# Performance work log

Hardware: AMD Instinct MI355X
Metric: run time of the kernel (lower is better)

## Reference

```python
import jax, jax.numpy as jnp
import numpy as np

N, T, D = 64, 2048, 256


def setup_inputs() -> dict:
    key = jax.random.key(0)
    k1, k2, k3, k4 = jax.random.split(key, 4)
    query = jax.random.normal(k1, (N, D), dtype=jnp.float32)
    key_t = jax.random.normal(k2, (N, T, D), dtype=jnp.float32)
    value = jax.random.normal(k3, (N, T, D), dtype=jnp.float32)
    lens = jax.random.randint(k4, (N,), 1, T + 1, dtype=jnp.int64)  # valid lengths in [1, T]
    return {"query": query, "key": key_t, "value": value, "lens": lens}


def reference(query, key, value, lens):
    # energy[n, t] = <key[n, t, :], query[n, :]>
    energy = jnp.einsum("ntd,nd->nt", key, query)
    attention = jax.nn.softmax(energy, axis=1)  # [N, T]
    # mask out positions >= lens[n], then renormalize over valid positions
    attention_mask = (jnp.arange(T)[None, :] < lens[:, None]).astype(attention.dtype)
    mask_attention = attention * attention_mask
    norm_attention = mask_attention / jnp.sum(mask_attention, axis=1, keepdims=True)
    # context[n, d] = sum_t norm_attention[n, t] * value[n, t, d]
    context = jnp.einsum("nt,ntd->nd", norm_attention, value)
    return (context, norm_attention)
```

## Files before the change

### kernel.cpp

```cpp
#include <hip/hip_runtime.h>


#define N_B 64
#define T_S 2048
#define D_S 256
#define TPB 256
#define RC 64
#define NC (T_S / RC)

typedef __attribute__((ext_vector_type(4))) float f4;
typedef __attribute__((ext_vector_type(2))) float f2;

__device__ __forceinline__ f4 ntload4(const float* p) {
  return __builtin_nontemporal_load((const f4*)p);
}
__device__ __forceinline__ f4 fma4(float s, f4 a, f4 b) {
  b.x = fmaf(s, a.x, b.x);
  b.y = fmaf(s, a.y, b.y);
  b.z = fmaf(s, a.z, b.z);
  b.w = fmaf(s, a.w, b.w);
  return b;
}

__global__ __launch_bounds__(TPB) void fused_kernel(
    const float* __restrict__ q, const float* __restrict__ k,
    const float* __restrict__ v, const int* __restrict__ lens,
    float* __restrict__ p_out, float2* __restrict__ mzc,
    float* __restrict__ Oc) {
  const int n = blockIdx.y, c = blockIdx.x;
  const int L = lens[n];
  const int t0 = c * RC;
  if (t0 >= L) return;
  const int tend = min(t0 + RC, L);
  const int tid = threadIdx.x;
  const int lane = tid & 63, wave = tid >> 6;

  __shared__ f4 q_sh[64];
  __shared__ float e_sh[RC];
  __shared__ float p_sh[RC];
  __shared__ f4 part[TPB];

  if (tid < 64) q_sh[tid] = ((const f4*)(q + (size_t)n * D_S))[tid];
  if (tid < RC) e_sh[tid] = -1e30f;
  __syncthreads();

  {
    const int s = lane & 15, qd = lane >> 4;
    const float* kb = k + (size_t)n * T_S * D_S + s * 4;
    const int rbase = t0 + wave * 16 + qd;
#pragma unroll
    for (int g = 0; g < 4; ++g) {
      const int r = rbase + g * 4;
      const float* krow = kb + (size_t)r * D_S;
      float acc = 0.f;
#pragma unroll
      for (int i = 0; i < 4; ++i) {
        const f4 kv = ntload4(krow + i * 64);
        const f4 qv = q_sh[i * 16 + s];
        acc = fmaf(kv.x, qv.x, acc);
        acc = fmaf(kv.y, qv.y, acc);
        acc = fmaf(kv.z, qv.z, acc);
        acc = fmaf(kv.w, qv.w, acc);
      }
#pragma unroll
      for (int off = 8; off > 0; off >>= 1) acc += __shfl_xor(acc, off, 64);
      if (s == 0 && r < tend) e_sh[r - t0] = acc;
    }
  }
  __syncthreads();

  if (wave == 0) {
    const float e = e_sh[lane];
    float m = e;
#pragma unroll
    for (int off = 32; off > 0; off >>= 1) m = fmaxf(m, __shfl_xor(m, off, 64));
    const float pv = __expf(e - m);
    float z = pv;
#pragma unroll
    for (int off = 32; off > 0; off >>= 1) z += __shfl_xor(z, off, 64);
    p_sh[lane] = pv;
    p_out[(size_t)n * T_S + t0 + lane] = pv;
    if (lane == 0) mzc[n * NC + c] = make_float2(m, z);
  }
  __syncthreads();

  const int dg = tid & 63, tg = tid >> 6;
  const float* vb = v + (size_t)n * T_S * D_S + (size_t)t0 * D_S + dg * 4;
  f4 a0 = {0.f, 0.f, 0.f, 0.f}, a1 = a0, a2 = a0, a3 = a0;
#pragma unroll
  for (int j = 0; j < 4; ++j) {
    const int r0 = j * 16 + tg;
    const f4 v0 = ntload4(vb + (size_t)r0 * D_S);
    const f4 v1 = ntload4(vb + (size_t)(r0 + 4) * D_S);
    const f4 v2 = ntload4(vb + (size_t)(r0 + 8) * D_S);
    const f4 v3 = ntload4(vb + (size_t)(r0 + 12) * D_S);
    a0 = fma4(p_sh[r0], v0, a0);
    a1 = fma4(p_sh[r0 + 4], v1, a1);
    a2 = fma4(p_sh[r0 + 8], v2, a2);
    a3 = fma4(p_sh[r0 + 12], v3, a3);
  }
  part[tid] = (a0 + a1) + (a2 + a3);
  __syncthreads();
  if (tg == 0) {
    const f4 r = part[dg] + part[dg + 64] + part[dg + 128] + part[dg + 192];
    ((f4*)(Oc + ((size_t)(n * NC + c)) * D_S))[dg] = r;
  }
}

__global__ __launch_bounds__(TPB) void merge_kernel(
    const int* __restrict__ lens, const float* __restrict__ p_in,
    const float2* __restrict__ mzc, const float* __restrict__ Oc,
    float* __restrict__ out_ctx, float* __restrict__ out_attn) {
  const int n = blockIdx.y, cx = blockIdx.x;
  const int L = lens[n];
  const int nc = (L + RC - 1) / RC;
  const int tid = threadIdx.x;
  __shared__ float s_sh[NC];
  __shared__ float cpart[TPB];

  if (tid < 64) {
    float m = -1e30f, z = 0.f;
    if (tid < nc) {
      const float2 mz = mzc[n * NC + tid];
      m = mz.x;
      z = mz.y;
    }
    float M = m;
#pragma unroll
    for (int off = 32; off > 0; off >>= 1) M = fmaxf(M, __shfl_xor(M, off, 64));
    const float sc = __expf(m - M);
    float zs = z * sc;
#pragma unroll
    for (int off = 32; off > 0; off >>= 1) zs += __shfl_xor(zs, off, 64);
    if (tid < NC) s_sh[tid] = sc / zs;
  }
  __syncthreads();

  {
    const int t = cx * (T_S / 4) + tid * 2;
    const f2 p = *(const f2*)(p_in + (size_t)n * T_S + t);
    const float sc = s_sh[t >> 6];
    f2 a;
    a.x = (t < L) ? p.x * sc : 0.f;
    a.y = (t + 1 < L) ? p.y * sc : 0.f;
    *(f2*)(out_attn + (size_t)n * T_S + t) = a;
  }

  {
    const int d = cx * 64 + (tid & 63);
    const int cg = tid >> 6;
    const float* ob = Oc + (size_t)n * NC * D_S + d;
    float acc = 0.f;
#pragma unroll
    for (int kk = 0; kk < 8; ++kk) {
      const int cc = cg + kk * 4;
      acc = fmaf(s_sh[cc], ob[(size_t)cc * D_S], acc);
    }
    cpart[tid] = acc;
    __syncthreads();
    if (tid < 64)
      out_ctx[(size_t)n * D_S + d] =
          (cpart[tid] + cpart[tid + 64]) + (cpart[tid + 128] + cpart[tid + 192]);
  }
}

extern "C" void kernel_launch(void* const* d_in, const int* in_sizes, int n_in,
                              void* d_out, int out_size, void* d_ws,
                              size_t ws_size, hipStream_t stream) {
  const float* query = (const float*)d_in[0];
  const float* key = (const float*)d_in[1];
  const float* value = (const float*)d_in[2];
  const int* lens = (const int*)d_in[3];

  float* out_ctx = (float*)d_out;
  float* out_attn = (float*)d_out + N_B * D_S;

  float* p = (float*)d_ws;
  float2* mzc = (float2*)(p + (size_t)N_B * T_S);
  float* Oc = (float*)(mzc + N_B * NC);

  const dim3 grid1(NC, N_B);
  fused_kernel<<<grid1, TPB, 0, stream>>>(query, key, value, lens, p, mzc, Oc);
  const dim3 grid2(4, N_B);
  merge_kernel<<<grid2, TPB, 0, stream>>>(lens, p, mzc, Oc, out_ctx, out_attn);
}
```

Baseline: 242.7 us.

## Make each wave own a 16-row chunk with wave-local softmax, no LDS or barriers

The fused kernel now gives each wavefront its own 16-row time chunk. The chunk's energies, local max/sum and weighted V accumulation stay in registers and use shuffles, so shared memory and block barriers are gone. Rows past the valid length skip their K loads, and V rows whose weight is zero are skipped. In exchange there are four times as many partial chunks, so the merge kernel handles 128 chunk partials per batch, which adds workspace traffic and reduction work.

Result: slower. 257.6 us (+6.1%).

```diff
diff --git a/kernel.cpp b/kernel.cpp
--- a/kernel.cpp
+++ b/kernel.cpp
@@ -5,8 +5,8 @@
 #define T_S 2048
 #define D_S 256
 #define TPB 256
-#define RC 64
-#define NC (T_S / RC)
+#define RC 16
+#define NCH (T_S / RC)
 
 typedef __attribute__((ext_vector_type(4))) float f4;
 typedef __attribute__((ext_vector_type(2))) float f2;
@@ -27,84 +27,91 @@
     const float* __restrict__ v, const int* __restrict__ lens,
     float* __restrict__ p_out, float2* __restrict__ mzc,
     float* __restrict__ Oc) {
-  const int n = blockIdx.y, c = blockIdx.x;
+  const int n = blockIdx.y;
   const int L = lens[n];
-  const int t0 = c * RC;
-  if (t0 >= L) return;
-  const int tend = min(t0 + RC, L);
-  const int tid = threadIdx.x;
-  const int lane = tid & 63, wave = tid >> 6;
-
-  __shared__ f4 q_sh[64];
-  __shared__ float e_sh[RC];
-  __shared__ float p_sh[RC];
-  __shared__ f4 part[TPB];
-
-  if (tid < 64) q_sh[tid] = ((const f4*)(q + (size_t)n * D_S))[tid];
-  if (tid < RC) e_sh[tid] = -1e30f;
-  __syncthreads();
-
-  {
-    const int s = lane & 15, qd = lane >> 4;
-    const float* kb = k + (size_t)n * T_S * D_S + s * 4;
-    const int rbase = t0 + wave * 16 + qd;
-#pragma unroll
-    for (int g = 0; g < 4; ++g) {
-      const int r = rbase + g * 4;
-      const float* krow = kb + (size_t)r * D_S;
-      float acc = 0.f;
-#pragma unroll
-      for (int i = 0; i < 4; ++i) {
-        const f4 kv = ntload4(krow + i * 64);
-        const f4 qv = q_sh[i * 16 + s];
-        acc = fmaf(kv.x, qv.x, acc);
-        acc = fmaf(kv.y, qv.y, acc);
-        acc = fmaf(kv.z, qv.z, acc);
-        acc = fmaf(kv.w, qv.w, acc);
-      }
-#pragma unroll
-      for (int off = 8; off > 0; off >>= 1) acc += __shfl_xor(acc, off, 64);
-      if (s == 0 && r < tend) e_sh[r - t0] = acc;
-    }
-  }
-  __syncthreads();
-
-  if (wave == 0) {
-    const float e = e_sh[lane];
-    float m = e;
-#pragma unroll
-    for (int off = 32; off > 0; off >>= 1) m = fmaxf(m, __shfl_xor(m, off, 64));
-    const float pv = __expf(e - m);
-    float z = pv;
-#pragma unroll
-    for (int off = 32; off > 0; off >>= 1) z += __shfl_xor(z, off, 64);
-    p_sh[lane] = pv;
-    p_out[(size_t)n * T_S + t0 + lane] = pv;
-    if (lane == 0) mzc[n * NC + c] = make_float2(m, z);
-  }
-  __syncthreads();
-
-  const int dg = tid & 63, tg = tid >> 6;
-  const float* vb = v + (size_t)n * T_S * D_S + (size_t)t0 * D_S + dg * 4;
-  f4 a0 = {0.f, 0.f, 0.f, 0.f}, a1 = a0, a2 = a0, a3 = a0;
-#pragma unroll
-  for (int j = 0; j < 4; ++j) {
-    const int r0 = j * 16 + tg;
-    const f4 v0 = ntload4(vb + (size_t)r0 * D_S);
-    const f4 v1 = ntload4(vb + (size_t)(r0 + 4) * D_S);
-    const f4 v2 = ntload4(vb + (size_t)(r0 + 8) * D_S);
-    const f4 v3 = ntload4(vb + (size_t)(r0 + 12) * D_S);
-    a0 = fma4(p_sh[r0], v0, a0);
-    a1 = fma4(p_sh[r0 + 4], v1, a1);
-    a2 = fma4(p_sh[r0 + 8], v2, a2);
-    a3 = fma4(p_sh[r0 + 12], v3, a3);
-  }
-  part[tid] = (a0 + a1) + (a2 + a3);
-  __syncthreads();
-  if (tg == 0) {
-    const f4 r = part[dg] + part[dg + 64] + part[dg + 128] + part[dg + 192];
-    ((f4*)(Oc + ((size_t)(n * NC + c)) * D_S))[dg] = r;
-  }
+  const int wave = threadIdx.x >> 6, lane = threadIdx.x & 63;
+  const int c16 = blockIdx.x * 4 + wave;
+  const int r0 = c16 * RC;
+  if (r0 >= L) return;
+  const int tendw = min(r0 + RC, L);
+  const int s = lane & 15, qd = lane >> 4;
+
+  const f4* qp = (const f4*)(q + (size_t)n * D_S);
+  const f4 qv0 = qp[s], qv1 = qp[s + 16], qv2 = qp[s + 32], qv3 = qp[s + 48];
+
+  const float* kb = k + (size_t)n * T_S * D_S + s * 4;
+  float e0 = -1e30f, e1 = -1e30f, e2 = -1e30f, e3 = -1e30f;
+#define EROW(G, EV)                                                      \
+  {                                                                      \
+    const int r = r0 + qd + 4 * (G);                                     \
+    if (r < tendw) {                                                     \
+      const float* krow = kb + (size_t)r * D_S;                          \
+      const f4 k0 = ntload4(krow);                                       \
+      const f4 k1 = ntload4(krow + 64);                                  \
+      const f4 k2 = ntload4(krow + 128);                                 \
+      const f4 k3 = ntload4(krow + 192);                                 \
+      float a = k0.x * qv0.x;                                            \
+      a = fmaf(k0.y, qv0.y, a);                                          \
+      a = fmaf(k0.z, qv0.z, a);                                          \
+      a = fmaf(k0.w, qv0.w, a);                                          \
+      a = fmaf(k1.x, qv1.x, a);                                          \
+      a = fmaf(k1.y, qv1.y, a);                                          \
+      a = fmaf(k1.z, qv1.z, a);                                          \
+      a = fmaf(k1.w, qv1.w, a);                                          \
+      a = fmaf(k2.x, qv2.x, a);                                          \
+      a = fmaf(k2.y, qv2.y, a);                                          \
+      a = fmaf(k2.z, qv2.z, a);                                          \
+      a = fmaf(k2.w, qv2.w, a);                                          \
+      a = fmaf(k3.x, qv3.x, a);                                          \
+      a = fmaf(k3.y, qv3.y, a);                                          \
+      a = fmaf(k3.z, qv3.z, a);                                          \
+      a = fmaf(k3.w, qv3.w, a);                                          \
+      a += __shfl_xor(a, 8, 64);                                         \
+      a += __shfl_xor(a, 4, 64);                                         \
+      a += __shfl_xor(a, 2, 64);                                         \
+      a += __shfl_xor(a, 1, 64);                                         \
+      EV = a;                                                            \
+    }                                                                    \
+  }
+  EROW(0, e0)
+  EROW(1, e1)
+  EROW(2, e2)
+  EROW(3, e3)
+#undef EROW
+
+  float m = fmaxf(fmaxf(e0, e1), fmaxf(e2, e3));
+  m = fmaxf(m, __shfl_xor(m, 16, 64));
+  m = fmaxf(m, __shfl_xor(m, 32, 64));
+  const float p0 = __expf(e0 - m), p1 = __expf(e1 - m);
+  const float p2 = __expf(e2 - m), p3 = __expf(e3 - m);
+  float z = (p0 + p1) + (p2 + p3);
+  z += __shfl_xor(z, 16, 64);
+  z += __shfl_xor(z, 32, 64);
+
+  if (s < 4) {
+    float pv = p0;
+    pv = (s == 1) ? p1 : pv;
+    pv = (s == 2) ? p2 : pv;
+    pv = (s == 3) ? p3 : pv;
+    p_out[(size_t)n * T_S + r0 + qd + 4 * s] = pv;
+  }
+  if (lane == 0) mzc[n * NCH + c16] = make_float2(m, z);
+
+  const float* vb = v + (size_t)n * T_S * D_S + (size_t)r0 * D_S + lane * 4;
+  f4 aA = {0.f, 0.f, 0.f, 0.f}, aB = aA;
+#define VROW(G, Q2, ACC)                                                   \
+  {                                                                       \
+    const float sc = __shfl(p##G, (Q2)*16, 64);       \
+    if (sc != 0.f)                                                        \
+      ACC = fma4(sc, ntload4(vb + (size_t)((Q2) + 4 * (G)) * D_S), ACC);  \
+  }
+  VROW(0, 0, aA) VROW(0, 1, aB) VROW(0, 2, aA) VROW(0, 3, aB)
+  VROW(1, 0, aA) VROW(1, 1, aB) VROW(1, 2, aA) VROW(1, 3, aB)
+  VROW(2, 0, aA) VROW(2, 1, aB) VROW(2, 2, aA) VROW(2, 3, aB)
+  VROW(3, 0, aA) VROW(3, 1, aB) VROW(3, 2, aA) VROW(3, 3, aB)
+#undef VROW
+
+  ((f4*)(Oc + ((size_t)(n * NCH + c16)) * D_S))[lane] = aA + aB;
 }
 
 __global__ __launch_bounds__(TPB) void merge_kernel(
@@ -115,51 +122,58 @@
   const int L = lens[n];
   const int nc = (L + RC - 1) / RC;
   const int tid = threadIdx.x;
-  __shared__ float s_sh[NC];
+  __shared__ float s_sh[NCH];
   __shared__ float cpart[TPB];
 
   if (tid < 64) {
-    float m = -1e30f, z = 0.f;
+    float m0 = -1e30f, z0 = 0.f, m1 = -1e30f, z1 = 0.f;
     if (tid < nc) {
-      const float2 mz = mzc[n * NC + tid];
-      m = mz.x;
-      z = mz.y;
+      const float2 a = mzc[n * NCH + tid];
+      m0 = a.x;
+      z0 = a.y;
     }
-    float M = m;
+    if (tid + 64 < nc) {
+      const float2 a = mzc[n * NCH + tid + 64];
+      m1 = a.x;
+      z1 = a.y;
+    }
+    float M = fmaxf(m0, m1);
 #pragma unroll
     for (int off = 32; off > 0; off >>= 1) M = fmaxf(M, __shfl_xor(M, off, 64));
-    const float sc = __expf(m - M);
-    float zs = z * sc;
+    const float sc0 = __expf(m0 - M), sc1 = __expf(m1 - M);
+    float zs = fmaf(z0, sc0, z1 * sc1);
 #pragma unroll
     for (int off = 32; off > 0; off >>= 1) zs += __shfl_xor(zs, off, 64);
-    if (tid < NC) s_sh[tid] = sc / zs;
+    const float inv = 1.f / zs;
+    s_sh[tid] = sc0 * inv;
+    s_sh[tid + 64] = sc1 * inv;
   }
   __syncthreads();
 
   {
     const int t = cx * (T_S / 4) + tid * 2;
-    const f2 p = *(const f2*)(p_in + (size_t)n * T_S + t);
-    const float sc = s_sh[t >> 6];
+    const f2 pp = *(const f2*)(p_in + (size_t)n * T_S + t);
+    const float sc = s_sh[t >> 4];
     f2 a;
-    a.x = (t < L) ? p.x * sc : 0.f;
-    a.y = (t + 1 < L) ? p.y * sc : 0.f;
+    a.x = (t < L) ? pp.x * sc : 0.f;
+    a.y = (t + 1 < L) ? pp.y * sc : 0.f;
     *(f2*)(out_attn + (size_t)n * T_S + t) = a;
   }
 
   {
     const int d = cx * 64 + (tid & 63);
     const int cg = tid >> 6;
-    const float* ob = Oc + (size_t)n * NC * D_S + d;
+    const float* ob = Oc + (size_t)n * NCH * D_S + d;
     float acc = 0.f;
 #pragma unroll
-    for (int kk = 0; kk < 8; ++kk) {
-      const int cc = cg + kk * 4;
-      acc = fmaf(s_sh[cc], ob[(size_t)cc * D_S], acc);
+    for (int kk = 0; kk < 32; ++kk) {
+      const int cc = cg * 32 + kk;
+      if (cc < nc) acc = fmaf(s_sh[cc], ob[(size_t)cc * D_S], acc);
     }
     cpart[tid] = acc;
     __syncthreads();
     if (tid < 64)
-      out_ctx[(size_t)n * D_S + d] =
+      out_ctx[(size_t)n * D_S + cx * 64 + tid] =
           (cpart[tid] + cpart[tid + 64]) + (cpart[tid + 128] + cpart[tid + 192]);
   }
 }
@@ -177,9 +191,9 @@
 
   float* p = (float*)d_ws;
   float2* mzc = (float2*)(p + (size_t)N_B * T_S);
-  float* Oc = (float*)(mzc + N_B * NC);
-
-  const dim3 grid1(NC, N_B);
+  float* Oc = (float*)(mzc + N_B * NCH);
+
+  const dim3 grid1(NCH / 4, N_B);
   fused_kernel<<<grid1, TPB, 0, stream>>>(query, key, value, lens, p, mzc, Oc);
   const dim3 grid2(4, N_B);
   merge_kernel<<<grid2, TPB, 0, stream>>>(lens, p, mzc, Oc, out_ctx, out_attn);
```

## Prefetch V chunk into LDS via async DMA while computing scores

Applied to the files above, without the earlier changes.

Issues all K loads into registers up front and starts asynchronous global-to-LDS loads of the V chunk before the dot products, so the V fetch overlaps the score computation and softmax instead of following them. Every wave now computes the chunk softmax redundantly and broadcasts p via shuffles, which removes the p_sh buffer and one barrier. The merge kernel now skips chunks beyond the valid length instead of reading unwritten Oc entries. The 64KB V tile in LDS lowers occupancy per CU, and the loop has no wait or barrier on the LDS DMA before V is read from LDS, so correctness depends on the barrier after the score stage.

New measurement: 246.6 us. Within noise of the previous version (+1.6%).

```diff
diff --git a/kernel.cpp b/kernel.cpp
--- a/kernel.cpp
+++ b/kernel.cpp
@@ -20,6 +20,11 @@
   b.z = fmaf(s, a.z, b.z);
   b.w = fmaf(s, a.w, b.w);
   return b;
+}
+__device__ __forceinline__ void ldsdma16(float* lds, const float* g) {
+  __builtin_amdgcn_global_load_lds(
+      (const __attribute__((address_space(1))) void*)g,
+      (__attribute__((address_space(3))) void*)lds, 16, 0, 0);
 }
 
 __global__ __launch_bounds__(TPB) void fused_kernel(
@@ -34,76 +39,105 @@
   const int tend = min(t0 + RC, L);
   const int tid = threadIdx.x;
   const int lane = tid & 63, wave = tid >> 6;
-
-  __shared__ f4 q_sh[64];
+  const int s = lane & 15, qd = lane >> 4;
+
+  __shared__ float v_sh[RC * D_S];
   __shared__ float e_sh[RC];
-  __shared__ float p_sh[RC];
   __shared__ f4 part[TPB];
 
-  if (tid < 64) q_sh[tid] = ((const f4*)(q + (size_t)n * D_S))[tid];
-  if (tid < RC) e_sh[tid] = -1e30f;
+  const f4* qp = (const f4*)(q + (size_t)n * D_S);
+  const f4 qv0 = qp[s], qv1 = qp[s + 16], qv2 = qp[s + 32], qv3 = qp[s + 48];
+
+  const float* kb =
+      k + (size_t)n * T_S * D_S + (size_t)(t0 + wave * 16) * D_S + s * 4;
+  f4 kr[4][4];
+#pragma unroll
+  for (int g = 0; g < 4; ++g) {
+    const float* krow = kb + (size_t)(qd + 4 * g) * D_S;
+#pragma unroll
+    for (int i = 0; i < 4; ++i) kr[g][i] = ntload4(krow + i * 64);
+  }
+
+  {
+    const float* vsrc =
+        v + (size_t)n * T_S * D_S + (size_t)(t0 + wave * 16) * D_S + lane * 4;
+    float* vdst = v_sh + wave * 16 * D_S;
+#pragma unroll
+    for (int i = 0; i < 16; ++i) ldsdma16(vdst + i * D_S, vsrc + (size_t)i * D_S);
+  }
+  __builtin_amdgcn_sched_barrier(0);
+
+  float e0, e1, e2, e3;
+#define EDOT(G, EV)                                                  \
+  {                                                                  \
+    float a = kr[G][0].x * qv0.x;                                    \
+    a = fmaf(kr[G][0].y, qv0.y, a);                                  \
+    a = fmaf(kr[G][0].z, qv0.z, a);                                  \
+    a = fmaf(kr[G][0].w, qv0.w, a);                                  \
+    a = fmaf(kr[G][1].x, qv1.x, a);                                  \
+    a = fmaf(kr[G][1].y, qv1.y, a);                                  \
+    a = fmaf(kr[G][1].z, qv1.z, a);                                  \
+    a = fmaf(kr[G][1].w, qv1.w, a);                                  \
+    a = fmaf(kr[G][2].x, qv2.x, a);                                  \
+    a = fmaf(kr[G][2].y, qv2.y, a);                                  \
+    a = fmaf(kr[G][2].z, qv2.z, a);                                  \
+    a = fmaf(kr[G][2].w, qv2.w, a);                                  \
+    a = fmaf(kr[G][3].x, qv3.x, a);                                  \
+    a = fmaf(kr[G][3].y, qv3.y, a);                                  \
+    a = fmaf(kr[G][3].z, qv3.z, a);                                  \
+    a = fmaf(kr[G][3].w, qv3.w, a);                                  \
+    a += __shfl_xor(a, 8, 64);                                       \
+    a += __shfl_xor(a, 4, 64);                                       \
+    a += __shfl_xor(a, 2, 64);                                       \
+    a += __shfl_xor(a, 1, 64);                                       \
+    EV = (t0 + wave * 16 + qd + 4 * (G) < tend) ? a : -1e30f;        \
+  }
+  EDOT(0, e0)
+  EDOT(1, e1)
+  EDOT(2, e2)
+  EDOT(3, e3)
+#undef EDOT
+
+  if (s == 0) {
+    e_sh[wave * 16 + qd] = e0;
+    e_sh[wave * 16 + qd + 4] = e1;
+    e_sh[wave * 16 + qd + 8] = e2;
+    e_sh[wave * 16 + qd + 12] = e3;
+  }
   __syncthreads();
 
-  {
-    const int s = lane & 15, qd = lane >> 4;
-    const float* kb = k + (size_t)n * T_S * D_S + s * 4;
-    const int rbase = t0 + wave * 16 + qd;
-#pragma unroll
-    for (int g = 0; g < 4; ++g) {
-      const int r = rbase + g * 4;
-      const float* krow = kb + (size_t)r * D_S;
-      float acc = 0.f;
-#pragma unroll
-      for (int i = 0; i < 4; ++i) {
-        const f4 kv = ntload4(krow + i * 64);
-        const f4 qv = q_sh[i * 16 + s];
-        acc = fmaf(kv.x, qv.x, acc);
-        acc = fmaf(kv.y, qv.y, acc);
-        acc = fmaf(kv.z, qv.z, acc);
-        acc = fmaf(kv.w, qv.w, acc);
-      }
-#pragma unroll
-      for (int off = 8; off > 0; off >>= 1) acc += __shfl_xor(acc, off, 64);
-      if (s == 0 && r < tend) e_sh[r - t0] = acc;
-    }
-  }
-  __syncthreads();
+  const float ee = e_sh[lane];
+  float m = ee;
+#pragma unroll
+  for (int off = 32; off > 0; off >>= 1) m = fmaxf(m, __shfl_xor(m, off, 64));
+  const float pv = __expf(ee - m);
+  float z = pv;
+#pragma unroll
+  for (int off = 32; off > 0; off >>= 1) z += __shfl_xor(z, off, 64);
 
   if (wave == 0) {
-    const float e = e_sh[lane];
-    float m = e;
-#pragma unroll
-    for (int off = 32; off > 0; off >>= 1) m = fmaxf(m, __shfl_xor(m, off, 64));
-    const float pv = __expf(e - m);
-    float z = pv;
-#pragma unroll
-    for (int off = 32; off > 0; off >>= 1) z += __shfl_xor(z, off, 64);
-    p_sh[lane] = pv;
     p_out[(size_t)n * T_S + t0 + lane] = pv;
     if (lane == 0) mzc[n * NC + c] = make_float2(m, z);
   }
-  __syncthreads();
-
-  const int dg = tid & 63, tg = tid >> 6;
-  const float* vb = v + (size_t)n * T_S * D_S + (size_t)t0 * D_S + dg * 4;
+
   f4 a0 = {0.f, 0.f, 0.f, 0.f}, a1 = a0, a2 = a0, a3 = a0;
 #pragma unroll
   for (int j = 0; j < 4; ++j) {
-    const int r0 = j * 16 + tg;
-    const f4 v0 = ntload4(vb + (size_t)r0 * D_S);
-    const f4 v1 = ntload4(vb + (size_t)(r0 + 4) * D_S);
-    const f4 v2 = ntload4(vb + (size_t)(r0 + 8) * D_S);
-    const f4 v3 = ntload4(vb + (size_t)(r0 + 12) * D_S);
-    a0 = fma4(p_sh[r0], v0, a0);
-    a1 = fma4(p_sh[r0 + 4], v1, a1);
-    a2 = fma4(p_sh[r0 + 8], v2, a2);
-    a3 = fma4(p_sh[r0 + 12], v3, a3);
+    const int r0 = j * 16 + wave;
+    const f4 v0 = *(const f4*)(v_sh + (size_t)r0 * D_S + lane * 4);
+    const f4 v1 = *(const f4*)(v_sh + (size_t)(r0 + 4) * D_S + lane * 4);
+    const f4 v2 = *(const f4*)(v_sh + (size_t)(r0 + 8) * D_S + lane * 4);
+    const f4 v3 = *(const f4*)(v_sh + (size_t)(r0 + 12) * D_S + lane * 4);
+    a0 = fma4(__shfl(pv, r0, 64), v0, a0);
+    a1 = fma4(__shfl(pv, r0 + 4, 64), v1, a1);
+    a2 = fma4(__shfl(pv, r0 + 8, 64), v2, a2);
+    a3 = fma4(__shfl(pv, r0 + 12, 64), v3, a3);
   }
   part[tid] = (a0 + a1) + (a2 + a3);
   __syncthreads();
-  if (tg == 0) {
-    const f4 r = part[dg] + part[dg + 64] + part[dg + 128] + part[dg + 192];
-    ((f4*)(Oc + ((size_t)(n * NC + c)) * D_S))[dg] = r;
+  if (wave == 0) {
+    const f4 r = part[lane] + part[lane + 64] + part[lane + 128] + part[lane + 192];
+    ((f4*)(Oc + ((size_t)(n * NC + c)) * D_S))[lane] = r;
   }
 }
 
@@ -154,7 +188,7 @@
 #pragma unroll
     for (int kk = 0; kk < 8; ++kk) {
       const int cc = cg + kk * 4;
-      acc = fmaf(s_sh[cc], ob[(size_t)cc * D_S], acc);
+      if (cc < nc) acc = fmaf(s_sh[cc], ob[(size_t)cc * D_S], acc);
     }
     cpart[tid] = acc;
     __syncthreads();
```

## Remove q/p shared-memory staging, prefetch V before softmax, compute softmax redundantly per wave

Applied to the files above, without the earlier changes.

Query slices now go straight into registers instead of through shared memory. All four K row groups are loaded up front, and the first quarter of V rows is prefetched before the barrier so those loads overlap the score reduction. Every wave recomputes the chunk softmax from e_sh and broadcasts probabilities with lane shuffles rather than a p_sh array, which removes two __syncthreads. The merge kernel also skips chunk partials beyond the valid count; this guards reads of uninitialised workspace at the cost of a branch and extra register pressure.

After: 245.9 us. No clear change (+1.3%).

```diff
diff --git a/kernel.cpp b/kernel.cpp
--- a/kernel.cpp
+++ b/kernel.cpp
@@ -34,76 +34,92 @@
   const int tend = min(t0 + RC, L);
   const int tid = threadIdx.x;
   const int lane = tid & 63, wave = tid >> 6;
-
-  __shared__ f4 q_sh[64];
+  const int s = lane & 15, qd = lane >> 4;
+
   __shared__ float e_sh[RC];
-  __shared__ float p_sh[RC];
   __shared__ f4 part[TPB];
 
-  if (tid < 64) q_sh[tid] = ((const f4*)(q + (size_t)n * D_S))[tid];
-  if (tid < RC) e_sh[tid] = -1e30f;
+  const f4* qp = (const f4*)(q + (size_t)n * D_S);
+  const f4 qv0 = qp[s], qv1 = qp[s + 16], qv2 = qp[s + 32], qv3 = qp[s + 48];
+
+  const float* kb =
+      k + (size_t)n * T_S * D_S + (size_t)(t0 + wave * 16) * D_S + s * 4;
+#pragma unroll
+  for (int g = 0; g < 4; ++g) {
+    const int row = wave * 16 + qd + 4 * g;
+    const float* krow = kb + (size_t)(qd + 4 * g) * D_S;
+    const f4 k0 = ntload4(krow);
+    const f4 k1 = ntload4(krow + 64);
+    const f4 k2 = ntload4(krow + 128);
+    const f4 k3 = ntload4(krow + 192);
+    float a = k0.x * qv0.x;
+    a = fmaf(k0.y, qv0.y, a);
+    a = fmaf(k0.z, qv0.z, a);
+    a = fmaf(k0.w, qv0.w, a);
+    a = fmaf(k1.x, qv1.x, a);
+    a = fmaf(k1.y, qv1.y, a);
+    a = fmaf(k1.z, qv1.z, a);
+    a = fmaf(k1.w, qv1.w, a);
+    a = fmaf(k2.x, qv2.x, a);
+    a = fmaf(k2.y, qv2.y, a);
+    a = fmaf(k2.z, qv2.z, a);
+    a = fmaf(k2.w, qv2.w, a);
+    a = fmaf(k3.x, qv3.x, a);
+    a = fmaf(k3.y, qv3.y, a);
+    a = fmaf(k3.z, qv3.z, a);
+    a = fmaf(k3.w, qv3.w, a);
+    a += __shfl_xor(a, 8, 64);
+    a += __shfl_xor(a, 4, 64);
+    a += __shfl_xor(a, 2, 64);
+    a += __shfl_xor(a, 1, 64);
+    a = (t0 + row < tend) ? a : -1e30f;
+    if (s == 0) e_sh[row] = a;
+  }
+
+  const float* vb = v + (size_t)n * T_S * D_S + (size_t)t0 * D_S + lane * 4;
+  const f4 pv0 = ntload4(vb + (size_t)wave * D_S);
+  const f4 pv1 = ntload4(vb + (size_t)(wave + 4) * D_S);
+  const f4 pv2 = ntload4(vb + (size_t)(wave + 8) * D_S);
+  const f4 pv3 = ntload4(vb + (size_t)(wave + 12) * D_S);
+
   __syncthreads();
 
-  {
-    const int s = lane & 15, qd = lane >> 4;
-    const float* kb = k + (size_t)n * T_S * D_S + s * 4;
-    const int rbase = t0 + wave * 16 + qd;
-#pragma unroll
-    for (int g = 0; g < 4; ++g) {
-      const int r = rbase + g * 4;
-      const float* krow = kb + (size_t)r * D_S;
-      float acc = 0.f;
-#pragma unroll
-      for (int i = 0; i < 4; ++i) {
-        const f4 kv = ntload4(krow + i * 64);
-        const f4 qv = q_sh[i * 16 + s];
-        acc = fmaf(kv.x, qv.x, acc);
-        acc = fmaf(kv.y, qv.y, acc);
-        acc = fmaf(kv.z, qv.z, acc);
-        acc = fmaf(kv.w, qv.w, acc);
-      }
-#pragma unroll
-      for (int off = 8; off > 0; off >>= 1) acc += __shfl_xor(acc, off, 64);
-      if (s == 0 && r < tend) e_sh[r - t0] = acc;
-    }
-  }
-  __syncthreads();
+  const float ee = e_sh[lane];
+  float m = ee;
+#pragma unroll
+  for (int off = 32; off > 0; off >>= 1) m = fmaxf(m, __shfl_xor(m, off, 64));
+  const float pvs = __expf(ee - m);
+  float z = pvs;
+#pragma unroll
+  for (int off = 32; off > 0; off >>= 1) z += __shfl_xor(z, off, 64);
 
   if (wave == 0) {
-    const float e = e_sh[lane];
-    float m = e;
-#pragma unroll
-    for (int off = 32; off > 0; off >>= 1) m = fmaxf(m, __shfl_xor(m, off, 64));
-    const float pv = __expf(e - m);
-    float z = pv;
-#pragma unroll
-    for (int off = 32; off > 0; off >>= 1) z += __shfl_xor(z, off, 64);
-    p_sh[lane] = pv;
-    p_out[(size_t)n * T_S + t0 + lane] = pv;
+    p_out[(size_t)n * T_S + t0 + lane] = pvs;
     if (lane == 0) mzc[n * NC + c] = make_float2(m, z);
   }
-  __syncthreads();
-
-  const int dg = tid & 63, tg = tid >> 6;
-  const float* vb = v + (size_t)n * T_S * D_S + (size_t)t0 * D_S + dg * 4;
-  f4 a0 = {0.f, 0.f, 0.f, 0.f}, a1 = a0, a2 = a0, a3 = a0;
-#pragma unroll
-  for (int j = 0; j < 4; ++j) {
-    const int r0 = j * 16 + tg;
+
+  f4 a0 = fma4(__shfl(pvs, wave, 64), pv0, f4{0.f, 0.f, 0.f, 0.f});
+  f4 a1 = fma4(__shfl(pvs, wave + 4, 64), pv1, f4{0.f, 0.f, 0.f, 0.f});
+  f4 a2 = fma4(__shfl(pvs, wave + 8, 64), pv2, f4{0.f, 0.f, 0.f, 0.f});
+  f4 a3 = fma4(__shfl(pvs, wave + 12, 64), pv3, f4{0.f, 0.f, 0.f, 0.f});
+#pragma unroll
+  for (int j = 1; j < 4; ++j) {
+    const int r0 = j * 16 + wave;
     const f4 v0 = ntload4(vb + (size_t)r0 * D_S);
     const f4 v1 = ntload4(vb + (size_t)(r0 + 4) * D_S);
     const f4 v2 = ntload4(vb + (size_t)(r0 + 8) * D_S);
     const f4 v3 = ntload4(vb + (size_t)(r0 + 12) * D_S);
-    a0 = fma4(p_sh[r0], v0, a0);
-    a1 = fma4(p_sh[r0 + 4], v1, a1);
-    a2 = fma4(p_sh[r0 + 8], v2, a2);
-    a3 = fma4(p_sh[r0 + 12], v3, a3);
+    a0 = fma4(__shfl(pvs, r0, 64), v0, a0);
+    a1 = fma4(__shfl(pvs, r0 + 4, 64), v1, a1);
+    a2 = fma4(__shfl(pvs, r0 + 8, 64), v2, a2);
+    a3 = fma4(__shfl(pvs, r0 + 12, 64), v3, a3);
   }
   part[tid] = (a0 + a1) + (a2 + a3);
   __syncthreads();
-  if (tg == 0) {
-    const f4 r = part[dg] + part[dg + 64] + part[dg + 128] + part[dg + 192];
-    ((f4*)(Oc + ((size_t)(n * NC + c)) * D_S))[dg] = r;
+  if (wave == 0) {
+    const f4 r =
+        part[lane] + part[lane + 64] + part[lane + 128] + part[lane + 192];
+    ((f4*)(Oc + ((size_t)(n * NC + c)) * D_S))[lane] = r;
   }
 }
 
@@ -154,7 +170,7 @@
 #pragma unroll
     for (int kk = 0; kk < 8; ++kk) {
       const int cc = cg + kk * 4;
-      acc = fmaf(s_sh[cc], ob[(size_t)cc * D_S], acc);
+      if (cc < nc) acc = fmaf(s_sh[cc], ob[(size_t)cc * D_S], acc);
     }
     cpart[tid] = acc;
     __syncthreads();
```
